# Kernel optimization log

Hardware: AMD Instinct MI355X
Metric: run time of the kernel (lower is better)

Reference implementation:

```python
import jax, jax.numpy as jnp
import numpy as np

SELF = 32      # self_obs_dim
OBS = 16       # obstacle_obs_dim
L = 16         # cfg.num_landmarks
H = 256        # obstacle_hidden_size
HEADS = 8
ATT = 32
NA = 4         # num_agents
TAIL = 4 * 8 * 4  # 4*state_dim*num_oppo_obs


def _mlp2(x, w1, b1, w2, b2):
    return jnp.tanh(jnp.tanh(x @ w1 + b1) @ w2 + b2)


def setup_inputs() -> dict:
    key = jax.random.key(0)
    ks = jax.random.split(key, 8)
    B = 16384
    obs = jax.random.normal(ks[0], (B, 480), jnp.float32)

    def lin(k, fin, fout):
        return jax.random.normal(k, (fin, fout), jnp.float32) * 0.02

    return {
        "obs": obs,
        "enc_w1": lin(ks[1], SELF + OBS, H), "enc_b1": jnp.zeros((H,), jnp.float32),
        "enc_w2": lin(ks[2], H, H),          "enc_b2": jnp.zeros((H,), jnp.float32),
        "val_w1": lin(ks[3], H, H),          "val_b1": jnp.zeros((H,), jnp.float32),
        "val_w2": lin(ks[4], H, H),          "val_b2": jnp.zeros((H,), jnp.float32),
        "vals_w1": lin(ks[5], H, H),         "vals_b1": jnp.zeros((H,), jnp.float32),
        "vals_w2": lin(ks[6], H, H),         "vals_b2": jnp.zeros((H,), jnp.float32),
        "ln_g": jnp.ones((H,), jnp.float32), "ln_b": jnp.zeros((H,), jnp.float32),
        "all_neighbor_obs_size": 64,
        "batch_size": B,
        "num_groups": 4096,
    }


def reference(obs, enc_w1, enc_b1, enc_w2, enc_b2,
              val_w1, val_b1, val_w2, val_b2,
              vals_w1, vals_b1, vals_w2, vals_b2,
              ln_g, ln_b,
              all_neighbor_obs_size, batch_size, num_groups):
    # slice out obstacle observations and pair each with tiled self obs
    obs_obst = obs[:, SELF + all_neighbor_obs_size: obs.shape[1] - TAIL].reshape(-1, OBS)
    self_rep = jnp.tile(obs[:, :SELF], (L, 1))  # torch .repeat(L,1)
    x = jnp.concatenate([self_rep, obs_obst], axis=1)  # [N*L, SELF+OBS]

    emb = _mlp2(x, enc_w1, enc_b1, enc_w2, enc_b2)      # [N*L, H]
    k = emb.reshape(batch_size, -1, H)                  # [B, S, H]
    q = k.mean(axis=1)                                  # [B, H]
    v = _mlp2(emb, val_w1, val_b1, val_w2, val_b2).reshape(batch_size, -1, H)

    scores = jnp.einsum('bh,bsh->bs', q / np.float32(np.sqrt(H)), k)
    att = jax.nn.softmax(scores, axis=-1)
    obstacle_mean_embed = jnp.einsum('bs,bsh->bh', att, v)  # [B, H]

    ov = _mlp2(obstacle_mean_embed, vals_w1, vals_b1, vals_w2, vals_b2)
    mu = ov.mean(axis=-1, keepdims=True)
    var = ov.var(axis=-1, keepdims=True)
    ov = (ov - mu) / jnp.sqrt(var + 1e-6) * ln_g + ln_b  # layernorm eps=1e-6

    P = batch_size // num_groups
    qg = obstacle_mean_embed.reshape(num_groups, P, H).mean(axis=1)
    qg = qg.reshape(num_groups, HEADS, ATT)
    kg = obstacle_mean_embed.reshape(num_groups, P, HEADS, ATT)
    vg = ov.reshape(num_groups, P, HEADS, ATT)

    sc = jnp.einsum('gha,gpha->ghp', qg / np.float32(np.sqrt(ATT)), kg)
    a = jax.nn.softmax(sc, axis=-1)
    out = jnp.einsum('ghp,gpha->gha', a, vg).reshape(-1, HEADS * ATT)  # [G, H]

    obstacles_attention = jnp.tile(out, (NA, 1))  # repeat(num_agents, 1)
    return (obstacles_attention, obstacle_mean_embed)
```

## Files before the change

kernel.cpp:

```cpp
#include <hip/hip_runtime.h>
#include <hip/hip_bf16.h>
#include <math.h>

#define BATCH   16384
#define G_NUM   4096
#define NL      16
#define HD      256
#define OBSW    480
#define LDA     264

using bf16x8 = __attribute__((ext_vector_type(8))) short;
using f32x4  = __attribute__((ext_vector_type(4))) float;

#define E1H 0
#define E1L 16384
#define E2H 32768
#define E2L 98304
#define V1H 163840
#define V1L 229376
#define V2H 294912
#define V2L 360448
#define PACK_ELEMS 425984

__device__ __forceinline__ float fast_tanh(float x) {
  float e = __expf(2.0f * x);
  return 1.0f - 2.0f * __builtin_amdgcn_rcpf(e + 1.0f);
}

__device__ __forceinline__ unsigned short f32_to_bf16(float x) {
  unsigned u = __float_as_uint(x);
  return (unsigned short)((u + 0x7fffu + ((u >> 16) & 1u)) >> 16);
}
__device__ __forceinline__ float bf16_to_f32(unsigned short h) {
  return __uint_as_float(((unsigned)h) << 16);
}
__device__ __forceinline__ void split_bf16(float x, unsigned short& hi, unsigned short& lo) {
  hi = f32_to_bf16(x);
  lo = f32_to_bf16(x - bf16_to_f32(hi));
}

__global__ void k_pack(const float* __restrict__ ew1, const float* __restrict__ ew2,
                       const float* __restrict__ vw1, const float* __restrict__ vw2,
                       unsigned short* __restrict__ wpk) {
  int bid = blockIdx.x, lane = threadIdx.x;
  const float* W; int KS, K, baseh, basel;
  if (bid < 32)       { W = ew1; KS = 2; K = 48;  baseh = E1H; basel = E1L; }
  else if (bid < 160) { W = ew2; KS = 8; K = 256; baseh = E2H; basel = E2L; bid -= 32; }
  else if (bid < 288) { W = vw1; KS = 8; K = 256; baseh = V1H; basel = V1L; bid -= 160; }
  else                { W = vw2; KS = 8; K = 256; baseh = V2H; basel = V2L; bid -= 288; }
  int t = bid & 15, ks = bid >> 4;
  int g = lane >> 4, c = t * 16 + (lane & 15);
  unsigned short hv[8], lv[8];
#pragma unroll
  for (int i = 0; i < 8; ++i) {
    int k = ks * 32 + g * 8 + i;
    float v = (k < K) ? W[k * HD + c] : 0.f;
    split_bf16(v, hv[i], lv[i]);
  }
  size_t off = ((size_t)(t * KS + ks) * 64 + lane) * 8;
#pragma unroll
  for (int i = 0; i < 8; ++i) { wpk[baseh + off + i] = hv[i]; wpk[basel + off + i] = lv[i]; }
}

template<int KS>
__device__ __forceinline__ void mfma_layer8(const unsigned short* Ahi, const unsigned short* Alo,
                                            const unsigned short* __restrict__ Bhi,
                                            const unsigned short* __restrict__ Blo,
                                            const float* __restrict__ bias,
                                            int w, int lane, f32x4 acc[4][2]) {
  const int m16 = lane & 15, g = lane >> 4;
#pragma unroll
  for (int nt2 = 0; nt2 < 2; ++nt2) {
    float b = bias[(2 * w + nt2) * 16 + m16];
#pragma unroll
    for (int mt = 0; mt < 4; ++mt) {
      acc[mt][nt2][0] = b; acc[mt][nt2][1] = b; acc[mt][nt2][2] = b; acc[mt][nt2][3] = b;
    }
  }
#pragma unroll 2
  for (int ks = 0; ks < KS; ++ks) {
    bf16x8 ah[4], al[4];
#pragma unroll
    for (int mt = 0; mt < 4; ++mt) {
      int off = (16 * mt + m16) * LDA + ks * 32 + 8 * g;
      ah[mt] = *(const bf16x8*)(Ahi + off);
      al[mt] = *(const bf16x8*)(Alo + off);
    }
#pragma unroll
    for (int nt2 = 0; nt2 < 2; ++nt2) {
      size_t foff = ((size_t)((2 * w + nt2) * KS + ks) * 64 + lane) * 8;
      bf16x8 bh = *(const bf16x8*)(Bhi + foff);
      bf16x8 bl = *(const bf16x8*)(Blo + foff);
#pragma unroll
      for (int mt = 0; mt < 4; ++mt) {
        acc[mt][nt2] = __builtin_amdgcn_mfma_f32_16x16x32_bf16(ah[mt], bh, acc[mt][nt2], 0, 0, 0);
        acc[mt][nt2] = __builtin_amdgcn_mfma_f32_16x16x32_bf16(ah[mt], bl, acc[mt][nt2], 0, 0, 0);
        acc[mt][nt2] = __builtin_amdgcn_mfma_f32_16x16x32_bf16(al[mt], bh, acc[mt][nt2], 0, 0, 0);
      }
    }
  }
}

__device__ __forceinline__ void store_acts8(f32x4 acc[4][2], unsigned short* Ahi,
                                            unsigned short* Alo, int w, int lane) {
  const int m16 = lane & 15, g = lane >> 4;
#pragma unroll
  for (int mt = 0; mt < 4; ++mt)
#pragma unroll
    for (int nt2 = 0; nt2 < 2; ++nt2) {
      int col = (2 * w + nt2) * 16 + m16;
#pragma unroll
      for (int r = 0; r < 4; ++r) {
        int row = 16 * mt + 4 * g + r;
        unsigned short h, l;
        split_bf16(fast_tanh(acc[mt][nt2][r]), h, l);
        Ahi[row * LDA + col] = h;
        Alo[row * LDA + col] = l;
      }
    }
}

__device__ __forceinline__ void block_reduce16(float part[NL], float* red, int tid) {
#pragma unroll
  for (int d = 1; d < 64; d <<= 1) {
#pragma unroll
    for (int s = 0; s < NL; ++s) part[s] += __shfl_xor(part[s], d, 64);
  }
  __syncthreads();
  if ((tid & 63) == 0) {
    int w = tid >> 6;
#pragma unroll
    for (int s = 0; s < NL; ++s) red[w * NL + s] = part[s];
  }
  __syncthreads();
}

__global__ __launch_bounds__(512, 4) void k_main(
    const float* __restrict__ obs,
    const float* __restrict__ eb1, const float* __restrict__ eb2,
    const float* __restrict__ vb1, const float* __restrict__ vb2,
    const unsigned short* __restrict__ wpk,
    float* __restrict__ ome_out) {
  __shared__ __align__(16) unsigned short Ahi[64 * LDA];
  __shared__ __align__(16) unsigned short Alo[64 * LDA];
  __shared__ float att_lds[4 * NL];

  const int tid = threadIdx.x;
  const int w = tid >> 6, lane = tid & 63;
  const int b = blockIdx.x;

#pragma unroll
  for (int r = 0; r < 4; ++r) {
    int e = r * 512 + tid, m = e >> 5, c = e & 31;
    int srow = (64 * b + m) & (BATCH - 1);
    unsigned short h, l; split_bf16(obs[srow * OBSW + c], h, l);
    Ahi[m * LDA + c] = h; Alo[m * LDA + c] = l;
  }
#pragma unroll
  for (int r = 0; r < 2; ++r) {
    int e = r * 512 + tid, m = e >> 4, kk = e & 15;
    float v = obs[(4 * b + (m >> 4)) * OBSW + 96 + 16 * (m & 15) + kk];
    unsigned short h, l; split_bf16(v, h, l);
    Ahi[m * LDA + 32 + kk] = h; Alo[m * LDA + 32 + kk] = l;
  }
#pragma unroll
  for (int r = 0; r < 2; ++r) {
    int e = r * 512 + tid, m = e >> 4, kk = e & 15;
    Ahi[m * LDA + 48 + kk] = 0; Alo[m * LDA + 48 + kk] = 0;
  }
  __syncthreads();

  f32x4 acc[4][2];

  mfma_layer8<2>(Ahi, Alo, wpk + E1H, wpk + E1L, eb1, w, lane, acc);
  __syncthreads();
  store_acts8(acc, Ahi, Alo, w, lane);
  __syncthreads();

  mfma_layer8<8>(Ahi, Alo, wpk + E2H, wpk + E2L, eb2, w, lane, acc);
  __syncthreads();
  store_acts8(acc, Ahi, Alo, w, lane);
  __syncthreads();

  if (w < 4) {
    const int p = w;
    float part[NL];
#pragma unroll
    for (int s = 0; s < NL; ++s) part[s] = 0.f;
#pragma unroll
    for (int cc = 0; cc < 4; ++cc) {
      int c = cc * 64 + lane;
      float ev[NL], qs = 0.f;
#pragma unroll
      for (int s = 0; s < NL; ++s) {
        int row = 16 * p + s;
        ev[s] = bf16_to_f32(Ahi[row * LDA + c]) + bf16_to_f32(Alo[row * LDA + c]);
        qs += ev[s];
      }
#pragma unroll
      for (int s = 0; s < NL; ++s) part[s] += qs * ev[s];
    }
#pragma unroll
    for (int d = 1; d < 64; d <<= 1) {
#pragma unroll
      for (int s = 0; s < NL; ++s) part[s] += __shfl_xor(part[s], d, 64);
    }
    float sc[NL], mx = -1e30f;
#pragma unroll
    for (int s = 0; s < NL; ++s) {
      sc[s] = part[s] * (1.0f / 256.0f);
      mx = fmaxf(mx, sc[s]);
    }
    float se = 0.f, at[NL];
#pragma unroll
    for (int s = 0; s < NL; ++s) { at[s] = expf(sc[s] - mx); se += at[s]; }
    float inv = 1.0f / se;
    if (lane == 0) {
#pragma unroll
      for (int s = 0; s < NL; ++s) att_lds[p * NL + s] = at[s] * inv;
    }
  }

  mfma_layer8<8>(Ahi, Alo, wpk + V1H, wpk + V1L, vb1, w, lane, acc);
  __syncthreads();
  store_acts8(acc, Ahi, Alo, w, lane);
  __syncthreads();

  mfma_layer8<8>(Ahi, Alo, wpk + V2H, wpk + V2L, vb2, w, lane, acc);
  __syncthreads();
  store_acts8(acc, Ahi, Alo, w, lane);
  __syncthreads();

  {
    int col = tid & 255, p0 = tid >> 8;
#pragma unroll
    for (int pp = 0; pp < 2; ++pp) {
      int p = p0 + 2 * pp;
      float o = 0.f;
#pragma unroll
      for (int s = 0; s < NL; ++s) {
        int row = 16 * p + s;
        float vv = bf16_to_f32(Ahi[row * LDA + col]) + bf16_to_f32(Alo[row * LDA + col]);
        o += att_lds[p * NL + s] * vv;
      }
      ome_out[(size_t)(4 * b + p) * HD + col] = o;
    }
  }
}

#define PADW 20
template<int K>
__device__ __forceinline__ void qgemm_read(const float* inT, const float* __restrict__ W,
                                           const float* __restrict__ bias,
                                           int jq, int sq, float acc[4][4]) {
  {
    const float4 bb = *(const float4*)(bias + 4 * jq);
    const float b4[4] = {bb.x, bb.y, bb.z, bb.w};
#pragma unroll
    for (int si = 0; si < 4; ++si)
#pragma unroll
      for (int ji = 0; ji < 4; ++ji) acc[si][ji] = b4[ji];
  }
  const float* arow = inT + 4 * sq;
  const float* wrow = W + 4 * jq;
#pragma unroll 4
  for (int k = 0; k < K; ++k) {
    const float4 av = *(const float4*)(arow + k * PADW);
    const float4 wv = *(const float4*)(wrow + (size_t)k * HD);
    const float a4[4] = {av.x, av.y, av.z, av.w};
    const float w4[4] = {wv.x, wv.y, wv.z, wv.w};
#pragma unroll
    for (int si = 0; si < 4; ++si)
#pragma unroll
      for (int ji = 0; ji < 4; ++ji) acc[si][ji] = fmaf(a4[si], w4[ji], acc[si][ji]);
  }
}
__device__ __forceinline__ void write_tile_tanh(float* outT, int jq, int sq,
                                                const float acc[4][4]) {
#pragma unroll
  for (int ji = 0; ji < 4; ++ji) {
    float4 o;
    o.x = fast_tanh(acc[0][ji]); o.y = fast_tanh(acc[1][ji]);
    o.z = fast_tanh(acc[2][ji]); o.w = fast_tanh(acc[3][ji]);
    *(float4*)(outT + (4 * jq + ji) * PADW + 4 * sq) = o;
  }
}
__device__ __forceinline__ void read_col16(const float* buf, int j, float v[NL]) {
  const float4* p = (const float4*)(buf + j * PADW);
  float4 a0 = p[0], a1 = p[1], a2 = p[2], a3 = p[3];
  v[0]=a0.x; v[1]=a0.y; v[2]=a0.z; v[3]=a0.w; v[4]=a1.x; v[5]=a1.y; v[6]=a1.z; v[7]=a1.w;
  v[8]=a2.x; v[9]=a2.y; v[10]=a2.z; v[11]=a2.w; v[12]=a3.x; v[13]=a3.y; v[14]=a3.z; v[15]=a3.w;
}
__global__ __launch_bounds__(256, 8) void k_vals(
    const float* __restrict__ ome,
    const float* __restrict__ w1, const float* __restrict__ b1,
    const float* __restrict__ w2, const float* __restrict__ b2,
    const float* __restrict__ lng, const float* __restrict__ lnb,
    float* __restrict__ ov) {
  __shared__ __align__(16) float buf[HD * PADW];
  __shared__ float red[4 * NL];
  const int j = threadIdx.x, jq = j >> 2, sq = j & 3;
  const int r0 = blockIdx.x * NL;
#pragma unroll
  for (int i = 0; i < NL; ++i) {
    int e = i * 256 + j, r = e >> 8, k = e & 255;
    buf[k * PADW + r] = ome[(size_t)(r0 + r) * HD + k];
  }
  __syncthreads();
  float acc[4][4];
  qgemm_read<HD>(buf, w1, b1, jq, sq, acc);
  __syncthreads();
  write_tile_tanh(buf, jq, sq, acc);
  __syncthreads();
  qgemm_read<HD>(buf, w2, b2, jq, sq, acc);
  __syncthreads();
  write_tile_tanh(buf, jq, sq, acc);
  __syncthreads();
  float o0[NL];
  read_col16(buf, j, o0);
  float part[NL];
#pragma unroll
  for (int s = 0; s < NL; ++s) part[s] = o0[s];
  block_reduce16(part, red, j);
  float mu[NL];
#pragma unroll
  for (int s = 0; s < NL; ++s)
    mu[s] = (red[s] + red[NL + s] + red[2 * NL + s] + red[3 * NL + s]) * (1.0f / 256.0f);
#pragma unroll
  for (int s = 0; s < NL; ++s) { float d = o0[s] - mu[s]; part[s] = d * d; }
  block_reduce16(part, red, j);
  float gv = lng[j], bv = lnb[j];
#pragma unroll
  for (int s = 0; s < NL; ++s) {
    float var = (red[s] + red[NL + s] + red[2 * NL + s] + red[3 * NL + s]) * (1.0f / 256.0f);
    ov[(size_t)(r0 + s) * HD + j] = (o0[s] - mu[s]) * rsqrtf(var + 1e-6f) * gv + bv;
  }
}

__global__ __launch_bounds__(256) void k_group(
    const float* __restrict__ ome,
    const float* __restrict__ ov,
    float* __restrict__ out) {
  const int g = blockIdx.x, j = threadIdx.x;
  float m[4], o[4];
#pragma unroll
  for (int p = 0; p < 4; ++p) {
    m[p] = ome[(size_t)(g * 4 + p) * HD + j];
    o[p] = ov[(size_t)(g * 4 + p) * HD + j];
  }
  float qv = (m[0] + m[1] + m[2] + m[3]) * 0.25f * 0.17677669529663687f;
  float sc[4];
#pragma unroll
  for (int p = 0; p < 4; ++p) {
    float t = qv * m[p];
#pragma unroll
    for (int d = 1; d < 32; d <<= 1) t += __shfl_xor(t, d, 64);
    sc[p] = t;
  }
  float mx = fmaxf(fmaxf(sc[0], sc[1]), fmaxf(sc[2], sc[3]));
  float e[4], se = 0.f;
#pragma unroll
  for (int p = 0; p < 4; ++p) { e[p] = expf(sc[p] - mx); se += e[p]; }
  float inv = 1.0f / se, r = 0.f;
#pragma unroll
  for (int p = 0; p < 4; ++p) r += e[p] * inv * o[p];
#pragma unroll
  for (int rep = 0; rep < 4; ++rep) out[(size_t)(rep * G_NUM + g) * HD + j] = r;
}

extern "C" void kernel_launch(void* const* d_in, const int* in_sizes, int n_in,
                              void* d_out, int out_size, void* d_ws, size_t ws_size,
                              hipStream_t stream) {
  const float* obs = (const float*)d_in[0];
  const float* ew1 = (const float*)d_in[1];
  const float* eb1 = (const float*)d_in[2];
  const float* ew2 = (const float*)d_in[3];
  const float* eb2 = (const float*)d_in[4];
  const float* vw1 = (const float*)d_in[5];
  const float* vb1 = (const float*)d_in[6];
  const float* vw2 = (const float*)d_in[7];
  const float* vb2 = (const float*)d_in[8];
  const float* sw1 = (const float*)d_in[9];
  const float* sb1 = (const float*)d_in[10];
  const float* sw2 = (const float*)d_in[11];
  const float* sb2 = (const float*)d_in[12];
  const float* lng = (const float*)d_in[13];
  const float* lnb = (const float*)d_in[14];

  float* out = (float*)d_out;
  float* ome = out + (size_t)BATCH * HD;
  float* ov  = (float*)d_ws;

  const size_t OV_BYTES = (size_t)BATCH * HD * 4;
  const size_t PACK_BYTES = (size_t)PACK_ELEMS * 2;
  unsigned short* wpk;
  if (ws_size >= OV_BYTES + PACK_BYTES)
    wpk = (unsigned short*)((char*)d_ws + OV_BYTES);
  else
    wpk = (unsigned short*)d_out;

  k_pack<<<416, 64, 0, stream>>>(ew1, ew2, vw1, vw2, wpk);
  k_main<<<G_NUM, 512, 0, stream>>>(obs, eb1, eb2, vb1, vb2, wpk, ome);
  k_vals<<<BATCH / NL, 256, 0, stream>>>(ome, sw1, sb1, sw2, sb2, lng, lnb, ov);
  k_group<<<G_NUM, 256, 0, stream>>>(ome, ov, out);
}
```

Measured before the change: 510.3 us.

## Move vals MLP to split-bf16 MFMA kernel and use truncating bf16 split

Replaces the scalar fp32 FMA k_vals kernel with an MFMA-based kernel. It packs the vals weights into hi/lo bf16 pairs and reuses the 3-product split-bf16 matmul, now templated on the number of row tiles. LayerNorm is rewritten as per-row shuffle reductions over 16 lanes. The bf16 hi/lo split also changes from round-to-nearest to truncation, which saves a few integer ops per element but loses a little accuracy in the low part.

```diff
diff --git a/kernel.cpp b/kernel.cpp
--- a/kernel.cpp
+++ b/kernel.cpp
@@ -20,7 +20,11 @@
 #define V1L 229376
 #define V2H 294912
 #define V2L 360448
-#define PACK_ELEMS 425984
+#define S1H 425984
+#define S1L 491520
+#define S2H 557056
+#define S2L 622592
+#define PACK_ELEMS 688128
 
 __device__ __forceinline__ float fast_tanh(float x) {
   float e = __expf(2.0f * x);
@@ -38,16 +42,25 @@
   hi = f32_to_bf16(x);
   lo = f32_to_bf16(x - bf16_to_f32(hi));
 }
+__device__ __forceinline__ void split_trunc(float x, unsigned short& hi, unsigned short& lo) {
+  unsigned u = __float_as_uint(x);
+  float hif = __uint_as_float(u & 0xffff0000u);
+  hi = (unsigned short)(u >> 16);
+  lo = (unsigned short)(__float_as_uint(x - hif) >> 16);
+}
 
 __global__ void k_pack(const float* __restrict__ ew1, const float* __restrict__ ew2,
                        const float* __restrict__ vw1, const float* __restrict__ vw2,
+                       const float* __restrict__ sw1, const float* __restrict__ sw2,
                        unsigned short* __restrict__ wpk) {
   int bid = blockIdx.x, lane = threadIdx.x;
   const float* W; int KS, K, baseh, basel;
   if (bid < 32)       { W = ew1; KS = 2; K = 48;  baseh = E1H; basel = E1L; }
   else if (bid < 160) { W = ew2; KS = 8; K = 256; baseh = E2H; basel = E2L; bid -= 32; }
   else if (bid < 288) { W = vw1; KS = 8; K = 256; baseh = V1H; basel = V1L; bid -= 160; }
-  else                { W = vw2; KS = 8; K = 256; baseh = V2H; basel = V2L; bid -= 288; }
+  else if (bid < 416) { W = vw2; KS = 8; K = 256; baseh = V2H; basel = V2L; bid -= 288; }
+  else if (bid < 544) { W = sw1; KS = 8; K = 256; baseh = S1H; basel = S1L; bid -= 416; }
+  else                { W = sw2; KS = 8; K = 256; baseh = S2H; basel = S2L; bid -= 544; }
   int t = bid & 15, ks = bid >> 4;
   int g = lane >> 4, c = t * 16 + (lane & 15);
   unsigned short hv[8], lv[8];
@@ -62,26 +75,26 @@
   for (int i = 0; i < 8; ++i) { wpk[baseh + off + i] = hv[i]; wpk[basel + off + i] = lv[i]; }
 }
 
-template<int KS>
+template<int KS, int MT>
 __device__ __forceinline__ void mfma_layer8(const unsigned short* Ahi, const unsigned short* Alo,
                                             const unsigned short* __restrict__ Bhi,
                                             const unsigned short* __restrict__ Blo,
                                             const float* __restrict__ bias,
-                                            int w, int lane, f32x4 acc[4][2]) {
+                                            int w, int lane, f32x4 acc[MT][2]) {
   const int m16 = lane & 15, g = lane >> 4;
 #pragma unroll
   for (int nt2 = 0; nt2 < 2; ++nt2) {
     float b = bias[(2 * w + nt2) * 16 + m16];
 #pragma unroll
-    for (int mt = 0; mt < 4; ++mt) {
+    for (int mt = 0; mt < MT; ++mt) {
       acc[mt][nt2][0] = b; acc[mt][nt2][1] = b; acc[mt][nt2][2] = b; acc[mt][nt2][3] = b;
     }
   }
 #pragma unroll 2
   for (int ks = 0; ks < KS; ++ks) {
-    bf16x8 ah[4], al[4];
-#pragma unroll
-    for (int mt = 0; mt < 4; ++mt) {
+    bf16x8 ah[MT], al[MT];
+#pragma unroll
+    for (int mt = 0; mt < MT; ++mt) {
       int off = (16 * mt + m16) * LDA + ks * 32 + 8 * g;
       ah[mt] = *(const bf16x8*)(Ahi + off);
       al[mt] = *(const bf16x8*)(Alo + off);
@@ -92,7 +105,7 @@
       bf16x8 bh = *(const bf16x8*)(Bhi + foff);
       bf16x8 bl = *(const bf16x8*)(Blo + foff);
 #pragma unroll
-      for (int mt = 0; mt < 4; ++mt) {
+      for (int mt = 0; mt < MT; ++mt) {
         acc[mt][nt2] = __builtin_amdgcn_mfma_f32_16x16x32_bf16(ah[mt], bh, acc[mt][nt2], 0, 0, 0);
         acc[mt][nt2] = __builtin_amdgcn_mfma_f32_16x16x32_bf16(ah[mt], bl, acc[mt][nt2], 0, 0, 0);
         acc[mt][nt2] = __builtin_amdgcn_mfma_f32_16x16x32_bf16(al[mt], bh, acc[mt][nt2], 0, 0, 0);
@@ -101,11 +114,12 @@
   }
 }
 
-__device__ __forceinline__ void store_acts8(f32x4 acc[4][2], unsigned short* Ahi,
+template<int MT>
+__device__ __forceinline__ void store_acts8(f32x4 acc[MT][2], unsigned short* Ahi,
                                             unsigned short* Alo, int w, int lane) {
   const int m16 = lane & 15, g = lane >> 4;
 #pragma unroll
-  for (int mt = 0; mt < 4; ++mt)
+  for (int mt = 0; mt < MT; ++mt)
 #pragma unroll
     for (int nt2 = 0; nt2 < 2; ++nt2) {
       int col = (2 * w + nt2) * 16 + m16;
@@ -113,26 +127,11 @@
       for (int r = 0; r < 4; ++r) {
         int row = 16 * mt + 4 * g + r;
         unsigned short h, l;
-        split_bf16(fast_tanh(acc[mt][nt2][r]), h, l);
+        split_trunc(fast_tanh(acc[mt][nt2][r]), h, l);
         Ahi[row * LDA + col] = h;
         Alo[row * LDA + col] = l;
       }
     }
-}
-
-__device__ __forceinline__ void block_reduce16(float part[NL], float* red, int tid) {
-#pragma unroll
-  for (int d = 1; d < 64; d <<= 1) {
-#pragma unroll
-    for (int s = 0; s < NL; ++s) part[s] += __shfl_xor(part[s], d, 64);
-  }
-  __syncthreads();
-  if ((tid & 63) == 0) {
-    int w = tid >> 6;
-#pragma unroll
-    for (int s = 0; s < NL; ++s) red[w * NL + s] = part[s];
-  }
-  __syncthreads();
 }
 
 __global__ __launch_bounds__(512, 4) void k_main(
@@ -153,14 +152,14 @@
   for (int r = 0; r < 4; ++r) {
     int e = r * 512 + tid, m = e >> 5, c = e & 31;
     int srow = (64 * b + m) & (BATCH - 1);
-    unsigned short h, l; split_bf16(obs[srow * OBSW + c], h, l);
+    unsigned short h, l; split_trunc(obs[srow * OBSW + c], h, l);
     Ahi[m * LDA + c] = h; Alo[m * LDA + c] = l;
   }
 #pragma unroll
   for (int r = 0; r < 2; ++r) {
     int e = r * 512 + tid, m = e >> 4, kk = e & 15;
     float v = obs[(4 * b + (m >> 4)) * OBSW + 96 + 16 * (m & 15) + kk];
-    unsigned short h, l; split_bf16(v, h, l);
+    unsigned short h, l; split_trunc(v, h, l);
     Ahi[m * LDA + 32 + kk] = h; Alo[m * LDA + 32 + kk] = l;
   }
 #pragma unroll
@@ -172,14 +171,14 @@
 
   f32x4 acc[4][2];
 
-  mfma_layer8<2>(Ahi, Alo, wpk + E1H, wpk + E1L, eb1, w, lane, acc);
-  __syncthreads();
-  store_acts8(acc, Ahi, Alo, w, lane);
-  __syncthreads();
-
-  mfma_layer8<8>(Ahi, Alo, wpk + E2H, wpk + E2L, eb2, w, lane, acc);
-  __syncthreads();
-  store_acts8(acc, Ahi, Alo, w, lane);
+  mfma_layer8<2, 4>(Ahi, Alo, wpk + E1H, wpk + E1L, eb1, w, lane, acc);
+  __syncthreads();
+  store_acts8<4>(acc, Ahi, Alo, w, lane);
+  __syncthreads();
+
+  mfma_layer8<8, 4>(Ahi, Alo, wpk + E2H, wpk + E2L, eb2, w, lane, acc);
+  __syncthreads();
+  store_acts8<4>(acc, Ahi, Alo, w, lane);
   __syncthreads();
 
   if (w < 4) {
@@ -221,14 +220,14 @@
     }
   }
 
-  mfma_layer8<8>(Ahi, Alo, wpk + V1H, wpk + V1L, vb1, w, lane, acc);
-  __syncthreads();
-  store_acts8(acc, Ahi, Alo, w, lane);
-  __syncthreads();
-
-  mfma_layer8<8>(Ahi, Alo, wpk + V2H, wpk + V2L, vb2, w, lane, acc);
-  __syncthreads();
-  store_acts8(acc, Ahi, Alo, w, lane);
+  mfma_layer8<8, 4>(Ahi, Alo, wpk + V1H, wpk + V1L, vb1, w, lane, acc);
+  __syncthreads();
+  store_acts8<4>(acc, Ahi, Alo, w, lane);
+  __syncthreads();
+
+  mfma_layer8<8, 4>(Ahi, Alo, wpk + V2H, wpk + V2L, vb2, w, lane, acc);
+  __syncthreads();
+  store_acts8<4>(acc, Ahi, Alo, w, lane);
   __syncthreads();
 
   {
@@ -248,92 +247,59 @@
   }
 }
 
-#define PADW 20
-template<int K>
-__device__ __forceinline__ void qgemm_read(const float* inT, const float* __restrict__ W,
-                                           const float* __restrict__ bias,
-                                           int jq, int sq, float acc[4][4]) {
-  {
-    const float4 bb = *(const float4*)(bias + 4 * jq);
-    const float b4[4] = {bb.x, bb.y, bb.z, bb.w};
-#pragma unroll
-    for (int si = 0; si < 4; ++si)
-#pragma unroll
-      for (int ji = 0; ji < 4; ++ji) acc[si][ji] = b4[ji];
-  }
-  const float* arow = inT + 4 * sq;
-  const float* wrow = W + 4 * jq;
-#pragma unroll 4
-  for (int k = 0; k < K; ++k) {
-    const float4 av = *(const float4*)(arow + k * PADW);
-    const float4 wv = *(const float4*)(wrow + (size_t)k * HD);
-    const float a4[4] = {av.x, av.y, av.z, av.w};
-    const float w4[4] = {wv.x, wv.y, wv.z, wv.w};
-#pragma unroll
-    for (int si = 0; si < 4; ++si)
-#pragma unroll
-      for (int ji = 0; ji < 4; ++ji) acc[si][ji] = fmaf(a4[si], w4[ji], acc[si][ji]);
-  }
-}
-__device__ __forceinline__ void write_tile_tanh(float* outT, int jq, int sq,
-                                                const float acc[4][4]) {
-#pragma unroll
-  for (int ji = 0; ji < 4; ++ji) {
-    float4 o;
-    o.x = fast_tanh(acc[0][ji]); o.y = fast_tanh(acc[1][ji]);
-    o.z = fast_tanh(acc[2][ji]); o.w = fast_tanh(acc[3][ji]);
-    *(float4*)(outT + (4 * jq + ji) * PADW + 4 * sq) = o;
-  }
-}
-__device__ __forceinline__ void read_col16(const float* buf, int j, float v[NL]) {
-  const float4* p = (const float4*)(buf + j * PADW);
-  float4 a0 = p[0], a1 = p[1], a2 = p[2], a3 = p[3];
-  v[0]=a0.x; v[1]=a0.y; v[2]=a0.z; v[3]=a0.w; v[4]=a1.x; v[5]=a1.y; v[6]=a1.z; v[7]=a1.w;
-  v[8]=a2.x; v[9]=a2.y; v[10]=a2.z; v[11]=a2.w; v[12]=a3.x; v[13]=a3.y; v[14]=a3.z; v[15]=a3.w;
-}
-__global__ __launch_bounds__(256, 8) void k_vals(
+__global__ __launch_bounds__(512, 4) void k_vals_mm(
     const float* __restrict__ ome,
-    const float* __restrict__ w1, const float* __restrict__ b1,
-    const float* __restrict__ w2, const float* __restrict__ b2,
+    const float* __restrict__ sb1, const float* __restrict__ sb2,
     const float* __restrict__ lng, const float* __restrict__ lnb,
+    const unsigned short* __restrict__ wpk,
     float* __restrict__ ov) {
-  __shared__ __align__(16) float buf[HD * PADW];
-  __shared__ float red[4 * NL];
-  const int j = threadIdx.x, jq = j >> 2, sq = j & 3;
-  const int r0 = blockIdx.x * NL;
-#pragma unroll
-  for (int i = 0; i < NL; ++i) {
-    int e = i * 256 + j, r = e >> 8, k = e & 255;
-    buf[k * PADW + r] = ome[(size_t)(r0 + r) * HD + k];
-  }
-  __syncthreads();
-  float acc[4][4];
-  qgemm_read<HD>(buf, w1, b1, jq, sq, acc);
-  __syncthreads();
-  write_tile_tanh(buf, jq, sq, acc);
-  __syncthreads();
-  qgemm_read<HD>(buf, w2, b2, jq, sq, acc);
-  __syncthreads();
-  write_tile_tanh(buf, jq, sq, acc);
-  __syncthreads();
-  float o0[NL];
-  read_col16(buf, j, o0);
-  float part[NL];
-#pragma unroll
-  for (int s = 0; s < NL; ++s) part[s] = o0[s];
-  block_reduce16(part, red, j);
-  float mu[NL];
-#pragma unroll
-  for (int s = 0; s < NL; ++s)
-    mu[s] = (red[s] + red[NL + s] + red[2 * NL + s] + red[3 * NL + s]) * (1.0f / 256.0f);
-#pragma unroll
-  for (int s = 0; s < NL; ++s) { float d = o0[s] - mu[s]; part[s] = d * d; }
-  block_reduce16(part, red, j);
-  float gv = lng[j], bv = lnb[j];
-#pragma unroll
-  for (int s = 0; s < NL; ++s) {
-    float var = (red[s] + red[NL + s] + red[2 * NL + s] + red[3 * NL + s]) * (1.0f / 256.0f);
-    ov[(size_t)(r0 + s) * HD + j] = (o0[s] - mu[s]) * rsqrtf(var + 1e-6f) * gv + bv;
+  __shared__ __align__(16) unsigned short Ahi[32 * LDA];
+  __shared__ __align__(16) unsigned short Alo[32 * LDA];
+
+  const int tid = threadIdx.x;
+  const int w = tid >> 6, lane = tid & 63;
+  const int b = blockIdx.x;
+
+#pragma unroll
+  for (int r = 0; r < 16; ++r) {
+    int e = r * 512 + tid, row = e >> 8, col = e & 255;
+    unsigned short h, l; split_trunc(ome[(size_t)(32 * b + row) * HD + col], h, l);
+    Ahi[row * LDA + col] = h; Alo[row * LDA + col] = l;
+  }
+  __syncthreads();
+
+  f32x4 acc[2][2];
+  mfma_layer8<8, 2>(Ahi, Alo, wpk + S1H, wpk + S1L, sb1, w, lane, acc);
+  __syncthreads();
+  store_acts8<2>(acc, Ahi, Alo, w, lane);
+  __syncthreads();
+  mfma_layer8<8, 2>(Ahi, Alo, wpk + S2H, wpk + S2L, sb2, w, lane, acc);
+  __syncthreads();
+  store_acts8<2>(acc, Ahi, Alo, w, lane);
+  __syncthreads();
+
+  const int row = tid >> 4, c0 = (tid & 15) * 16;
+  float v[16], s = 0.f;
+#pragma unroll
+  for (int i = 0; i < 16; ++i) {
+    int c = c0 + i;
+    v[i] = bf16_to_f32(Ahi[row * LDA + c]) + bf16_to_f32(Alo[row * LDA + c]);
+    s += v[i];
+  }
+#pragma unroll
+  for (int d = 1; d < 16; d <<= 1) s += __shfl_xor(s, d, 64);
+  float mu = s * (1.0f / 256.0f);
+  float q = 0.f;
+#pragma unroll
+  for (int i = 0; i < 16; ++i) { float dd = v[i] - mu; q += dd * dd; }
+#pragma unroll
+  for (int d = 1; d < 16; d <<= 1) q += __shfl_xor(q, d, 64);
+  float rsq = rsqrtf(q * (1.0f / 256.0f) + 1e-6f);
+#pragma unroll
+  for (int i = 0; i < 16; ++i) {
+    int c = c0 + i;
+    float y = (v[i] - mu) * rsq * lng[c] + lnb[c];
+    ov[(size_t)(32 * b + row) * HD + c] = y;
   }
 }
 
@@ -399,8 +365,8 @@
   else
     wpk = (unsigned short*)d_out;
 
-  k_pack<<<416, 64, 0, stream>>>(ew1, ew2, vw1, vw2, wpk);
+  k_pack<<<672, 64, 0, stream>>>(ew1, ew2, vw1, vw2, sw1, sw2, wpk);
   k_main<<<G_NUM, 512, 0, stream>>>(obs, eb1, eb2, vb1, vb2, wpk, ome);
-  k_vals<<<BATCH / NL, 256, 0, stream>>>(ome, sw1, sb1, sw2, sb2, lng, lnb, ov);
+  k_vals_mm<<<BATCH / 32, 512, 0, stream>>>(ome, sb1, sb2, lng, lnb, wpk, ov);
   k_group<<<G_NUM, 256, 0, stream>>>(ome, ov, out);
 }
```

Result: faster. 441.8 us (-13.4%).
